# Kernel tuning notes

Hardware: AMD Instinct MI355X
Metric: run time of the kernel (lower is better)

## Reference

```python
import jax, jax.numpy as jnp
import numpy as np

ALPHA = 0.9          # alpha_mem
THRESHOLD = 1.0
WINDOW = 1.0         # module-level `window`; spike fn receives threshold*window
MEM_SUBTRACT = THRESHOLD  # membrane_subtract defaults to threshold


@jax.custom_vjp
def spike(v):
    # sinabs ThresholdSubtract forward: multiple spikes per step via floor division
    return jnp.where(v > 0, jnp.floor(v / THRESHOLD), 0.0)

def _spike_fwd(v):
    return spike(v), v

def _spike_bwd(v, g):
    # surrogate gradient: boxcar heaviside(v - (threshold - window)) / threshold
    grad = (v >= (THRESHOLD - THRESHOLD * WINDOW)).astype(g.dtype) / THRESHOLD
    return (g * grad,)

spike.defvjp(_spike_fwd, _spike_bwd)


def setup_inputs() -> dict:
    key = jax.random.key(0)
    k1, k2 = jax.random.split(key, 2)
    B, T, N = 32, 1000, 1024
    input_current = jax.random.normal(k1, (B, T, N), dtype=jnp.float32)
    w_rec = jax.random.normal(k2, (N, N), dtype=jnp.float32) * 0.02  # Linear weight [out, in]
    b_rec = jnp.zeros((N,), dtype=jnp.float32)
    return {"input_current": input_current, "w_rec": w_rec, "b_rec": b_rec}


def reference(input_current, w_rec, b_rec):
    B, T, N = input_current.shape

    def step(carry, x_t):
        state, rec = carry                      # [B, N] each
        total = x_t + rec                       # recurrent feedback added to input
        act = spike(state)                      # spikes from state BEFORE integration (1-step delay)
        state = state - act * MEM_SUBTRACT      # membrane subtract after spiking
        state = state * ALPHA + (1.0 - ALPHA) * total  # leaky integration
        rec = act @ w_rec.T + b_rec             # recurrent GEMM for next step
        return (state, rec), act

    state0 = jnp.zeros((B, N), dtype=input_current.dtype)
    rec0 = jnp.zeros((B, N), dtype=input_current.dtype)
    xs = jnp.swapaxes(input_current, 0, 1)      # [T, B, N]
    _, spikes = jax.lax.scan(step, (state0, rec0), xs)
    return jnp.swapaxes(spikes, 0, 1)           # [B, T, N]
```

## Files before the change

### kernel.cpp

```cpp
#include <hip/hip_runtime.h>
#include <cstdint>
#include <cstddef>

#define B_       32
#define T_       1000
#define N_       1024
#define THREADS_ 256
#define WAVES_   4
#define CHUNK_   8
#define NCHUNK_  125
#define DEPTH_   4
#define SLOT_BYTES_ 32768
#define ZBLOCKS_ 2048

typedef float v4f __attribute__((ext_vector_type(4)));
typedef __attribute__((address_space(1))) const void gc_void;
typedef __attribute__((address_space(3))) void lds_void;

__device__ __forceinline__ void barrier_lds() {
  __asm__ volatile("s_waitcnt lgkmcnt(0)\n\ts_barrier" ::: "memory");
}

__device__ __forceinline__ v4f vmax4(v4f a, v4f b) {
  v4f r;
  r.x = fmaxf(a.x, b.x); r.y = fmaxf(a.y, b.y);
  r.z = fmaxf(a.z, b.z); r.w = fmaxf(a.w, b.w);
  return r;
}

#define DSRD(dst, base, imm)                                                 \
  asm volatile("ds_read_b128 %0, %1 offset:" #imm : "=v"(dst) : "v"(base))

#define ISSUE_DMA(cc)                                                        \
  do {                                                                       \
    const float* _g = xg + (size_t)(cc) * (CHUNK_ * N_);                     \
    char* _l = xls + ((cc) & (DEPTH_ - 1)) * SLOT_BYTES_;                    \
    __builtin_amdgcn_global_load_lds((gc_void*)(_g + 0 * N_), (lds_void*)(_l + 0 * 4096), 16, 0, 0); \
    __builtin_amdgcn_global_load_lds((gc_void*)(_g + 1 * N_), (lds_void*)(_l + 1 * 4096), 16, 0, 0); \
    __builtin_amdgcn_global_load_lds((gc_void*)(_g + 2 * N_), (lds_void*)(_l + 2 * 4096), 16, 0, 0); \
    __builtin_amdgcn_global_load_lds((gc_void*)(_g + 3 * N_), (lds_void*)(_l + 3 * 4096), 16, 0, 0); \
    __builtin_amdgcn_global_load_lds((gc_void*)(_g + 4 * N_), (lds_void*)(_l + 4 * 4096), 16, 0, 0); \
    __builtin_amdgcn_global_load_lds((gc_void*)(_g + 5 * N_), (lds_void*)(_l + 5 * 4096), 16, 0, 0); \
    __builtin_amdgcn_global_load_lds((gc_void*)(_g + 6 * N_), (lds_void*)(_l + 6 * 4096), 16, 0, 0); \
    __builtin_amdgcn_global_load_lds((gc_void*)(_g + 7 * N_), (lds_void*)(_l + 7 * 4096), 16, 0, 0); \
    __builtin_amdgcn_sched_barrier(0);           \
  } while (0)

#define SPEC_STEP(xf)                                                        \
  do {                                                                       \
    cmax = vmax4(cmax, st);                                                  \
    v4f _t = (xf) + rr;                                                      \
    st = st * 0.9f + 0.1f * _t;                                              \
    rr = brec;                                                               \
  } while (0)

#define PROCESS(cc, VM)                                                      \
  do {                                                                       \
    unsigned _a = xb + (unsigned)(((cc) & (DEPTH_ - 1)) * SLOT_BYTES_)       \
                     + ((unsigned)tid << 4);                                 \
    asm volatile("s_waitcnt vmcnt(" #VM ")" ::: "memory");                   \
    v4f _x0, _x1, _x2, _x3, _x4, _x5, _x6, _x7;                              \
    DSRD(_x0, _a, 0);     DSRD(_x1, _a, 4096);                               \
    DSRD(_x2, _a, 8192);  DSRD(_x3, _a, 12288);                              \
    DSRD(_x4, _a, 16384); DSRD(_x5, _a, 20480);                              \
    DSRD(_x6, _a, 24576); DSRD(_x7, _a, 28672);                              \
    asm volatile("s_waitcnt lgkmcnt(0)" ::: "memory");                       \
    __builtin_amdgcn_sched_barrier(0);    \
    v4f st = state, rr = rec, cmax = state;                                  \
    SPEC_STEP(_x0); SPEC_STEP(_x1); SPEC_STEP(_x2); SPEC_STEP(_x3);          \
    SPEC_STEP(_x4); SPEC_STEP(_x5); SPEC_STEP(_x6); SPEC_STEP(_x7);          \
    float _m = fmaxf(fmaxf(cmax.x, cmax.y), fmaxf(cmax.z, cmax.w));          \
    int _any = (_m >= 1.0f);                                                 \
    const int _p = (cc) & 1;                                                 \
    unsigned long long _wm = __ballot(_any);                                 \
    if (lane == 0) s_cmask[_p][wv] = _wm;                                    \
    barrier_lds();                                                           \
    unsigned long long _ab =                                                 \
        s_cmask[_p][0] | s_cmask[_p][1] | s_cmask[_p][2] | s_cmask[_p][3];   \
    if (_ab == 0ULL) { state = st; rec = brec; }                             \
    else { replay(cc); }                                                     \
  } while (0)

__global__ __launch_bounds__(THREADS_, 1)
void lif_fused(const float* __restrict__ x, const float* __restrict__ w,
               const float* __restrict__ brec_g, float* __restrict__ out,
               unsigned long long* __restrict__ ws_rec,
               unsigned int* __restrict__ ws_cnt, int cap)
{
  if (blockIdx.x >= B_) {
    const size_t n4 = (size_t)B_ * T_ * N_ / 4;
    size_t i = (size_t)(blockIdx.x - B_) * THREADS_ + threadIdx.x;
    const size_t stride = (size_t)(gridDim.x - B_) * THREADS_;
    v4f* o4 = (v4f*)out;
    v4f z = (v4f)(0.f);
    for (; i < n4; i += stride) __builtin_nontemporal_store(z, &o4[i]);
    return;
  }

  const int b    = blockIdx.x;
  const int tid  = threadIdx.x;
  const int lane = tid & 63;
  const int wv   = tid >> 6;
  const int n0   = tid << 2;

  __shared__ v4f xbuf4[DEPTH_ * CHUNK_ * N_ / 4];
  __shared__ unsigned long long s_cmask[2][WAVES_];
  __shared__ unsigned long long s_mask [2][WAVES_];
  __shared__ v4f                s_val  [2][THREADS_];
  __shared__ unsigned int       s_spkcnt;

  if (tid == 0) s_spkcnt = 0;

  const float* xg = x + (size_t)b * T_ * N_ + n0;
  char* xls = (char*)xbuf4 + (wv << 10);
  const unsigned xb = (unsigned)(uintptr_t)(__attribute__((address_space(3))) void*)xbuf4;

  v4f state = (v4f)(0.f);
  v4f rec   = (v4f)(0.f);
  const v4f brec = *(const v4f*)(brec_g + n0);

  auto replay = [&](int cc) {
    v4f st = state;
    v4f r  = rec;
    const float* xrep = xg + (size_t)cc * (CHUNK_ * N_);
#pragma unroll 1
    for (int k = 0; k < CHUNK_; ++k) {
      const int q = k & 1;
      v4f xv = *(const v4f*)(xrep + (size_t)k * N_);
      float tx = xv.x + r.x, ty = xv.y + r.y, tz = xv.z + r.z, tw = xv.w + r.w;
      float ax = (st.x > 0.f) ? floorf(st.x) : 0.f;
      float ay = (st.y > 0.f) ? floorf(st.y) : 0.f;
      float az = (st.z > 0.f) ? floorf(st.z) : 0.f;
      float aw = (st.w > 0.f) ? floorf(st.w) : 0.f;
      int ms = (ax != 0.f) | (ay != 0.f) | (az != 0.f) | (aw != 0.f);
      if (ms) {
        v4f v; v.x = ax; v.y = ay; v.z = az; v.w = aw;
        s_val[q][tid] = v;
        unsigned int off = (unsigned int)((cc * CHUNK_ + k) * N_ + n0);
        float av[4] = {ax, ay, az, aw};
#pragma unroll
        for (int e = 0; e < 4; ++e) {
          if (av[e] != 0.f) {
            unsigned int idx = atomicAdd(&s_spkcnt, 1u);
            if ((int)idx < cap)
              ws_rec[(size_t)b * cap + idx] =
                  ((unsigned long long)(off + e) << 32) |
                  (unsigned long long)__float_as_uint(av[e]);
          }
        }
      }
      unsigned long long sm = __ballot(ms);
      if (lane == 0) s_mask[q][wv] = sm;
      st.x = (st.x - ax) * 0.9f + 0.1f * tx;
      st.y = (st.y - ay) * 0.9f + 0.1f * ty;
      st.z = (st.z - az) * 0.9f + 0.1f * tz;
      st.w = (st.w - aw) * 0.9f + 0.1f * tw;
      barrier_lds();
      v4f racc = brec;
#pragma unroll 1
      for (int w2 = 0; w2 < WAVES_; ++w2) {
        unsigned long long mm = s_mask[q][w2];
        while (mm) {
          int l = __builtin_ctzll(mm);
          mm &= mm - 1;
          int j = (w2 << 6) + l;
          v4f v = s_val[q][j];
          int jn = j << 2;
          if (v.x != 0.f) {
            racc.x += v.x * w[(size_t)(n0 + 0) * N_ + jn];
            racc.y += v.x * w[(size_t)(n0 + 1) * N_ + jn];
            racc.z += v.x * w[(size_t)(n0 + 2) * N_ + jn];
            racc.w += v.x * w[(size_t)(n0 + 3) * N_ + jn];
          }
          if (v.y != 0.f) {
            int j1 = jn + 1;
            racc.x += v.y * w[(size_t)(n0 + 0) * N_ + j1];
            racc.y += v.y * w[(size_t)(n0 + 1) * N_ + j1];
            racc.z += v.y * w[(size_t)(n0 + 2) * N_ + j1];
            racc.w += v.y * w[(size_t)(n0 + 3) * N_ + j1];
          }
          if (v.z != 0.f) {
            int j2 = jn + 2;
            racc.x += v.z * w[(size_t)(n0 + 0) * N_ + j2];
            racc.y += v.z * w[(size_t)(n0 + 1) * N_ + j2];
            racc.z += v.z * w[(size_t)(n0 + 2) * N_ + j2];
            racc.w += v.z * w[(size_t)(n0 + 3) * N_ + j2];
          }
          if (v.w != 0.f) {
            int j3 = jn + 3;
            racc.x += v.w * w[(size_t)(n0 + 0) * N_ + j3];
            racc.y += v.w * w[(size_t)(n0 + 1) * N_ + j3];
            racc.z += v.w * w[(size_t)(n0 + 2) * N_ + j3];
            racc.w += v.w * w[(size_t)(n0 + 3) * N_ + j3];
          }
        }
      }
      r = racc;
    }
    state = st;
    rec   = r;
  };

  ISSUE_DMA(0); ISSUE_DMA(1); ISSUE_DMA(2);

#pragma unroll 1
  for (int c = 0; c < NCHUNK_ - 3; ++c) {
    ISSUE_DMA(c + 3);
    PROCESS(c, 24);
  }
  PROCESS(122, 16);
  PROCESS(123, 8);
  PROCESS(124, 0);

  __syncthreads();
  if (tid == 0) ws_cnt[b] = s_spkcnt;
}

__global__ void scatter_spikes(const unsigned long long* __restrict__ rec,
                               const unsigned int* __restrict__ cnt,
                               float* __restrict__ out, int cap)
{
  int b = blockIdx.x;
  unsigned int n = cnt[b];
  if ((int)n > cap) n = cap;
  for (unsigned int i = threadIdx.x; i < n; i += blockDim.x) {
    unsigned long long r = rec[(size_t)b * cap + i];
    unsigned int off = (unsigned int)(r >> 32);
    float v = __uint_as_float((unsigned int)r);
    out[(size_t)b * (T_ * N_) + off] = v;
  }
}

extern "C" void kernel_launch(void* const* d_in, const int* in_sizes, int n_in,
                              void* d_out, int out_size, void* d_ws, size_t ws_size,
                              hipStream_t stream) {
  const float* x  = (const float*)d_in[0];
  const float* w  = (const float*)d_in[1];
  const float* br = (const float*)d_in[2];
  float* out = (float*)d_out;

  int cap = 4096;
  size_t need = (size_t)B_ * cap * 8 + B_ * 4;
  if (ws_size < need && ws_size > 256)
    cap = (int)((ws_size - 256) / ((size_t)B_ * 8));
  unsigned long long* rec = (unsigned long long*)d_ws;
  unsigned int* cnt = (unsigned int*)((char*)d_ws + (size_t)B_ * cap * 8);

  lif_fused<<<B_ + ZBLOCKS_, THREADS_, 0, stream>>>(x, w, br, out, rec, cnt, cap);
  scatter_spikes<<<B_, THREADS_, 0, stream>>>(rec, cnt, out, cap);
}
```

Measured before the change: 405.4 us.

## Warp-specialize loads: producer waves fill LDS ring for compute waves

```diff
diff --git a/kernel.cpp b/kernel.cpp
--- a/kernel.cpp
+++ b/kernel.cpp
@@ -5,21 +5,15 @@
 #define B_       32
 #define T_       1000
 #define N_       1024
-#define THREADS_ 256
-#define WAVES_   4
+#define THREADS_ 512
+#define CWAVES_  4
 #define CHUNK_   8
 #define NCHUNK_  125
-#define DEPTH_   4
+#define DEPTH_   2
 #define SLOT_BYTES_ 32768
 #define ZBLOCKS_ 2048
 
 typedef float v4f __attribute__((ext_vector_type(4)));
-typedef __attribute__((address_space(1))) const void gc_void;
-typedef __attribute__((address_space(3))) void lds_void;
-
-__device__ __forceinline__ void barrier_lds() {
-  __asm__ volatile("s_waitcnt lgkmcnt(0)\n\ts_barrier" ::: "memory");
-}
 
 __device__ __forceinline__ v4f vmax4(v4f a, v4f b) {
   v4f r;
@@ -31,20 +25,8 @@
 #define DSRD(dst, base, imm)                                                 \
   asm volatile("ds_read_b128 %0, %1 offset:" #imm : "=v"(dst) : "v"(base))
 
-#define ISSUE_DMA(cc)                                                        \
-  do {                                                                       \
-    const float* _g = xg + (size_t)(cc) * (CHUNK_ * N_);                     \
-    char* _l = xls + ((cc) & (DEPTH_ - 1)) * SLOT_BYTES_;                    \
-    __builtin_amdgcn_global_load_lds((gc_void*)(_g + 0 * N_), (lds_void*)(_l + 0 * 4096), 16, 0, 0); \
-    __builtin_amdgcn_global_load_lds((gc_void*)(_g + 1 * N_), (lds_void*)(_l + 1 * 4096), 16, 0, 0); \
-    __builtin_amdgcn_global_load_lds((gc_void*)(_g + 2 * N_), (lds_void*)(_l + 2 * 4096), 16, 0, 0); \
-    __builtin_amdgcn_global_load_lds((gc_void*)(_g + 3 * N_), (lds_void*)(_l + 3 * 4096), 16, 0, 0); \
-    __builtin_amdgcn_global_load_lds((gc_void*)(_g + 4 * N_), (lds_void*)(_l + 4 * 4096), 16, 0, 0); \
-    __builtin_amdgcn_global_load_lds((gc_void*)(_g + 5 * N_), (lds_void*)(_l + 5 * 4096), 16, 0, 0); \
-    __builtin_amdgcn_global_load_lds((gc_void*)(_g + 6 * N_), (lds_void*)(_l + 6 * 4096), 16, 0, 0); \
-    __builtin_amdgcn_global_load_lds((gc_void*)(_g + 7 * N_), (lds_void*)(_l + 7 * 4096), 16, 0, 0); \
-    __builtin_amdgcn_sched_barrier(0);           \
-  } while (0)
+#define GLD(dst, p)                                                          \
+  asm volatile("global_load_dwordx4 %0, %1, off" : "=v"(dst) : "v"(p))
 
 #define SPEC_STEP(xf)                                                        \
   do {                                                                       \
@@ -54,17 +36,16 @@
     rr = brec;                                                               \
   } while (0)
 
-#define PROCESS(cc, VM)                                                      \
+#define PROCESS(cc)                                                          \
   do {                                                                       \
-    unsigned _a = xb + (unsigned)(((cc) & (DEPTH_ - 1)) * SLOT_BYTES_)       \
+    unsigned _a = xb + (unsigned)(((cc) & 1) * SLOT_BYTES_)                  \
                      + ((unsigned)tid << 4);                                 \
-    asm volatile("s_waitcnt vmcnt(" #VM ")" ::: "memory");                   \
     v4f _x0, _x1, _x2, _x3, _x4, _x5, _x6, _x7;                              \
     DSRD(_x0, _a, 0);     DSRD(_x1, _a, 4096);                               \
     DSRD(_x2, _a, 8192);  DSRD(_x3, _a, 12288);                              \
     DSRD(_x4, _a, 16384); DSRD(_x5, _a, 20480);                              \
     DSRD(_x6, _a, 24576); DSRD(_x7, _a, 28672);                              \
-    asm volatile("s_waitcnt lgkmcnt(0)" ::: "memory");                       \
+    asm volatile("s_waitcnt lgkmcnt(0)");                                    \
     __builtin_amdgcn_sched_barrier(0);    \
     v4f st = state, rr = rec, cmax = state;                                  \
     SPEC_STEP(_x0); SPEC_STEP(_x1); SPEC_STEP(_x2); SPEC_STEP(_x3);          \
@@ -74,7 +55,7 @@
     const int _p = (cc) & 1;                                                 \
     unsigned long long _wm = __ballot(_any);                                 \
     if (lane == 0) s_cmask[_p][wv] = _wm;                                    \
-    barrier_lds();                                                           \
+    __syncthreads();                                                         \
     unsigned long long _ab =                                                 \
         s_cmask[_p][0] | s_cmask[_p][1] | s_cmask[_p][2] | s_cmask[_p][3];   \
     if (_ab == 0ULL) { state = st; rec = brec; }                             \
@@ -101,19 +82,68 @@
   const int tid  = threadIdx.x;
   const int lane = tid & 63;
   const int wv   = tid >> 6;
-  const int n0   = tid << 2;
-
-  __shared__ v4f xbuf4[DEPTH_ * CHUNK_ * N_ / 4];
-  __shared__ unsigned long long s_cmask[2][WAVES_];
-  __shared__ unsigned long long s_mask [2][WAVES_];
-  __shared__ v4f                s_val  [2][THREADS_];
+
+  __shared__ v4f xring[DEPTH_][CHUNK_][N_ / 4];
+  __shared__ unsigned long long s_cmask[2][CWAVES_];
+  __shared__ unsigned long long s_mask [2][CWAVES_];
+  __shared__ v4f                s_val  [2][CWAVES_ * 64];
   __shared__ unsigned int       s_spkcnt;
 
   if (tid == 0) s_spkcnt = 0;
 
-  const float* xg = x + (size_t)b * T_ * N_ + n0;
-  char* xls = (char*)xbuf4 + (wv << 10);
-  const unsigned xb = (unsigned)(uintptr_t)(__attribute__((address_space(3))) void*)xbuf4;
+  const float* xg_base = x + (size_t)b * T_ * N_;
+
+  if (wv >= CWAVES_) {
+    const int pw  = wv - CWAVES_;
+    const int col = (pw << 6) + lane;
+    const float* sbase = xg_base + ((size_t)col << 2);
+    {
+      v4f a0, a1, a2, a3, a4, a5, a6, a7;
+      GLD(a0, sbase + 0 * N_); GLD(a1, sbase + 1 * N_);
+      GLD(a2, sbase + 2 * N_); GLD(a3, sbase + 3 * N_);
+      GLD(a4, sbase + 4 * N_); GLD(a5, sbase + 5 * N_);
+      GLD(a6, sbase + 6 * N_); GLD(a7, sbase + 7 * N_);
+      asm volatile("s_waitcnt vmcnt(0)" ::: "memory");
+      xring[0][0][col] = a0; xring[0][1][col] = a1;
+      xring[0][2][col] = a2; xring[0][3][col] = a3;
+      xring[0][4][col] = a4; xring[0][5][col] = a5;
+      xring[0][6][col] = a6; xring[0][7][col] = a7;
+    }
+    __syncthreads();
+#pragma unroll 1
+    for (int c = 0; c < NCHUNK_; ++c) {
+      if (c + 1 < NCHUNK_) {
+        const float* pg = sbase + (size_t)(c + 1) * (CHUNK_ * N_);
+        v4f a0, a1, a2, a3, a4, a5, a6, a7;
+        GLD(a0, pg + 0 * N_); GLD(a1, pg + 1 * N_);
+        GLD(a2, pg + 2 * N_); GLD(a3, pg + 3 * N_);
+        GLD(a4, pg + 4 * N_); GLD(a5, pg + 5 * N_);
+        GLD(a6, pg + 6 * N_); GLD(a7, pg + 7 * N_);
+        asm volatile("s_waitcnt vmcnt(0)" ::: "memory");
+        const int sl = (c + 1) & 1;
+        xring[sl][0][col] = a0; xring[sl][1][col] = a1;
+        xring[sl][2][col] = a2; xring[sl][3][col] = a3;
+        xring[sl][4][col] = a4; xring[sl][5][col] = a5;
+        xring[sl][6][col] = a6; xring[sl][7][col] = a7;
+      }
+      __syncthreads();
+      const int p = c & 1;
+      unsigned long long ab =
+          s_cmask[p][0] | s_cmask[p][1] | s_cmask[p][2] | s_cmask[p][3];
+      if (ab != 0ULL) {
+#pragma unroll 1
+        for (int k = 0; k < CHUNK_; ++k) __syncthreads();
+      }
+    }
+    __syncthreads();
+    return;
+  }
+
+  __builtin_amdgcn_s_setprio(1);
+  const int n0 = tid << 2;
+
+  const unsigned xb =
+      (unsigned)(uintptr_t)(__attribute__((address_space(3))) void*)xring;
 
   v4f state = (v4f)(0.f);
   v4f rec   = (v4f)(0.f);
@@ -122,11 +152,11 @@
   auto replay = [&](int cc) {
     v4f st = state;
     v4f r  = rec;
-    const float* xrep = xg + (size_t)cc * (CHUNK_ * N_);
+    const int sl = cc & 1;
 #pragma unroll 1
     for (int k = 0; k < CHUNK_; ++k) {
       const int q = k & 1;
-      v4f xv = *(const v4f*)(xrep + (size_t)k * N_);
+      v4f xv = xring[sl][k][tid];
       float tx = xv.x + r.x, ty = xv.y + r.y, tz = xv.z + r.z, tw = xv.w + r.w;
       float ax = (st.x > 0.f) ? floorf(st.x) : 0.f;
       float ay = (st.y > 0.f) ? floorf(st.y) : 0.f;
@@ -155,10 +185,10 @@
       st.y = (st.y - ay) * 0.9f + 0.1f * ty;
       st.z = (st.z - az) * 0.9f + 0.1f * tz;
       st.w = (st.w - aw) * 0.9f + 0.1f * tw;
-      barrier_lds();
+      __syncthreads();
       v4f racc = brec;
 #pragma unroll 1
-      for (int w2 = 0; w2 < WAVES_; ++w2) {
+      for (int w2 = 0; w2 < CWAVES_; ++w2) {
         unsigned long long mm = s_mask[q][w2];
         while (mm) {
           int l = __builtin_ctzll(mm);
@@ -201,16 +231,11 @@
     rec   = r;
   };
 
-  ISSUE_DMA(0); ISSUE_DMA(1); ISSUE_DMA(2);
-
-#pragma unroll 1
-  for (int c = 0; c < NCHUNK_ - 3; ++c) {
-    ISSUE_DMA(c + 3);
-    PROCESS(c, 24);
-  }
-  PROCESS(122, 16);
-  PROCESS(123, 8);
-  PROCESS(124, 0);
+  __syncthreads();
+#pragma unroll 1
+  for (int c = 0; c < NCHUNK_; ++c) {
+    PROCESS(c);
+  }
 
   __syncthreads();
   if (tid == 0) ws_cnt[b] = s_spkcnt;
```

After: 397.2 us. -2.0%, faster.
